# Kernel optimization log

Hardware: AMD Instinct MI355X
Metric: run time of the kernel (lower is better)

Reference implementation:

```python
import jax, jax.numpy as jnp
import numpy as np

N_NODES = 50000
N_EDGES = 1000000
H_DIM = 128
OUT_DIM = 64
N_RELS = 16  # num_bases == num_rels


def setup_inputs() -> dict:
    key = jax.random.key(0)
    ks = jax.random.split(key, 12)
    node_ids = jnp.arange(N_NODES, dtype=jnp.int64) if jax.config.jax_enable_x64 else jnp.arange(N_NODES, dtype=jnp.int32)
    src = jax.random.randint(ks[0], (N_EDGES,), 0, N_NODES)
    dst = jax.random.randint(ks[1], (N_EDGES,), 0, N_NODES)
    etype = jax.random.randint(ks[2], (N_EDGES,), 0, N_RELS)
    norm = jax.random.uniform(ks[3], (N_EDGES, 1), dtype=jnp.float32)
    s1 = 1.0 / np.sqrt(H_DIM)
    s2 = 1.0 / np.sqrt(OUT_DIM)
    emb = jax.random.normal(ks[4], (N_NODES, H_DIM), dtype=jnp.float32)
    V1 = jax.random.normal(ks[5], (N_RELS, H_DIM, H_DIM), dtype=jnp.float32) * s1
    comp1 = jax.random.normal(ks[6], (N_RELS, N_RELS), dtype=jnp.float32) * (1.0 / np.sqrt(N_RELS))
    bias1 = jnp.zeros((H_DIM,), dtype=jnp.float32)
    V2 = jax.random.normal(ks[7], (N_RELS, H_DIM, OUT_DIM), dtype=jnp.float32) * s2
    comp2 = jax.random.normal(ks[8], (N_RELS, N_RELS), dtype=jnp.float32) * (1.0 / np.sqrt(N_RELS))
    bias2 = jnp.zeros((OUT_DIM,), dtype=jnp.float32)
    return {"node_ids": node_ids, "src": src, "dst": dst, "etype": etype, "norm": norm,
            "emb": emb, "V1": V1, "comp1": comp1, "bias1": bias1,
            "V2": V2, "comp2": comp2, "bias2": bias2}


def _rel_graph_conv(x, src, dst, etype, norm, V, comp, bias, num_nodes):
    # Basis decomposition: W_r = sum_b comp[r, b] * V_b  -> [R, in, out]
    W = jnp.einsum('rb,bio->rio', comp, V)
    # Per-relation transform of all nodes: [R, N, out]
    Y = jnp.einsum('ni,rio->rno', x, W)
    # Per-edge message: gather (etype, src) then scale by norm  -> [E, out]
    m = Y[etype, src] * norm
    # Scatter-add to destination nodes
    h = jax.ops.segment_sum(m, dst, num_segments=num_nodes)
    return h + bias


def reference(node_ids, src, dst, etype, norm, emb, V1, comp1, bias1, V2, comp2, bias2):
    x = emb[node_ids]  # [N, H]
    h = jax.nn.relu(_rel_graph_conv(x, src, dst, etype, norm, V1, comp1, bias1, x.shape[0]))
    h = _rel_graph_conv(h, src, dst, etype, norm, V2, comp2, bias2, x.shape[0])
    return h
```

## Files before the change

kernel.cpp:

```cpp
#include <hip/hip_runtime.h>


typedef short bf16x8 __attribute__((ext_vector_type(8)));
typedef float f32x4 __attribute__((ext_vector_type(4)));

#define RELS 16
#define HDIM 128
#define DSTBLK 66
#define MT_P 5
#define CHUNK 32
#define MAXBINS 12288
#define MAXCH 96

__device__ inline unsigned short f2bf(float f) {
  unsigned int u = __float_as_uint(f);
  unsigned int r = u + 0x7FFFu + ((u >> 16) & 1u);
  return (unsigned short)(r >> 16);
}

__device__ inline void barrier_nodrain() {
  __builtin_amdgcn_sched_barrier(0);
  asm volatile("s_waitcnt lgkmcnt(0)" ::: "memory");
  __builtin_amdgcn_s_barrier();
  __builtin_amdgcn_sched_barrier(0);
}

__global__ void cvt_bf16(const float* __restrict__ in, unsigned short* __restrict__ out, int n8) {
  int i = blockIdx.x * blockDim.x + threadIdx.x;
  if (i >= n8) return;
  float4 a = ((const float4*)in)[i * 2];
  float4 b = ((const float4*)in)[i * 2 + 1];
  uint4 o;
  o.x = (unsigned)f2bf(a.x) | ((unsigned)f2bf(a.y) << 16);
  o.y = (unsigned)f2bf(a.z) | ((unsigned)f2bf(a.w) << 16);
  o.z = (unsigned)f2bf(b.x) | ((unsigned)f2bf(b.y) << 16);
  o.w = (unsigned)f2bf(b.z) | ((unsigned)f2bf(b.w) << 16);
  ((uint4*)out)[i] = o;
}

__global__ void compute_w(const float* __restrict__ comp, const float* __restrict__ V,
                          unsigned short* __restrict__ Wt, int IO) {
  int idx = blockIdx.x * blockDim.x + threadIdx.x;
  if (idx >= RELS * IO * HDIM) return;
  int k = idx & (HDIM - 1);
  int o = (idx >> 7) % IO;
  int r = idx / (IO * HDIM);
  float s = 0.f;
#pragma unroll
  for (int b = 0; b < RELS; b++)
    s = fmaf(comp[r * RELS + b], V[(size_t)b * HDIM * IO + (size_t)k * IO + o], s);
  Wt[idx] = f2bf(s);
}

__global__ void hist_bins(const int* __restrict__ dst, const int* __restrict__ etype,
                          int n, int nbins, int* __restrict__ counts) {
  __shared__ int lh[MAXBINS];
  for (int j = threadIdx.x; j < nbins; j += blockDim.x) lh[j] = 0;
  __syncthreads();
  for (int i = blockIdx.x * blockDim.x + threadIdx.x; i < n; i += gridDim.x * blockDim.x)
    atomicAdd(&lh[(dst[i] / DSTBLK) * RELS + etype[i]], 1);
  __syncthreads();
  for (int j = threadIdx.x; j < nbins; j += blockDim.x) {
    int c = lh[j];
    if (c) atomicAdd(&counts[j], c);
  }
}

__global__ void scan_offsets(const int* __restrict__ counts, int* __restrict__ offsets, int nbins) {
  __shared__ int csum[256];
  const int t = threadIdx.x;
  const int CH = (nbins + 255) / 256;
  int lo = t * CH, hi = min(lo + CH, nbins);
  int s = 0;
  for (int i = lo; i < hi; i++) s += (counts[i] + 15) & ~15;
  csum[t] = s;
  __syncthreads();
#pragma unroll
  for (int d = 1; d < 256; d <<= 1) {
    int v = (t >= d) ? csum[t - d] : 0;
    __syncthreads();
    csum[t] += v;
    __syncthreads();
  }
  int run = (t == 0) ? 0 : csum[t - 1];
  for (int i = lo; i < hi; i++) {
    offsets[i] = run;
    run += (counts[i] + 15) & ~15;
  }
  if (lo < nbins && hi == nbins) offsets[nbins] = run;
}

__global__ void scatter_bins(const int* __restrict__ src, const int* __restrict__ dst,
                             const int* __restrict__ etype, const float* __restrict__ norm,
                             int n, const int* __restrict__ offsets, int* __restrict__ cursor,
                             uint2* __restrict__ ebuf) {
  for (int i = blockIdx.x * blockDim.x + threadIdx.x; i < n; i += gridDim.x * blockDim.x) {
    int d = dst[i];
    int blk = d / DSTBLK;
    int b = blk * RELS + etype[i];
    int p = offsets[b] + atomicAdd(&cursor[b], 1);
    ebuf[p] = make_uint2((unsigned)src[i] | ((unsigned)(d - blk * DSTBLK) << 20),
                         __float_as_uint(norm[i]));
  }
}

template <int OUT, bool BF16_RELU_OUT>
__launch_bounds__(256, (OUT == 64) ? 4 : 3)
__global__ void rgcn_layer(const unsigned short* __restrict__ Xb,
                           const unsigned short* __restrict__ Wt,
                           const uint2* __restrict__ ebuf,
                           const int* __restrict__ offsets, const int* __restrict__ counts,
                           const float* __restrict__ bias, void* __restrict__ Hout,
                           int nNodes) {
  constexpr int NT = OUT / 64;
  __shared__ __align__(16) unsigned short xs[2][CHUNK][136];
  __shared__ __align__(16) unsigned short ys[OUT][40];
  __shared__ __align__(16) unsigned short pmat[2][80][40];
  __shared__ __align__(8) int2 descS[MAXCH];
  __shared__ int sBase[16], sCnt[16], sStart[17];

  const int t = threadIdx.x;
  const int w = t >> 6;
  const int lane = t & 63;
  const int quad = lane >> 4;
  const int l16 = lane & 15;
  const int r0 = t >> 4;
  const int k8 = t & 15;
  const bool isHandler = (t & 7) == 0;
  const int myCol = t >> 3;
  const int nodeBase = blockIdx.x * DSTBLK;
  const int binBase = blockIdx.x * RELS;
  const int colBase = w * (OUT / 4);

  for (int i = t; i < 2 * CHUNK * 136 / 8; i += 256) ((uint4*)xs)[i] = make_uint4(0, 0, 0, 0);
  for (int i = t; i < OUT * 40 / 8; i += 256) ((uint4*)ys)[i] = make_uint4(0, 0, 0, 0);
  for (int i = t; i < 2 * 80 * 40 / 8; i += 256) ((uint4*)pmat)[i] = make_uint4(0, 0, 0, 0);

  if (t < 16) {
    sBase[t] = offsets[binBase + t];
    sCnt[t] = counts[binBase + t];
  }
  __syncthreads();
  if (t == 0) {
    int run = 0;
#pragma unroll
    for (int b = 0; b < 16; b++) {
      sStart[b] = run;
      run += (sCnt[b] + CHUNK - 1) / CHUNK;
    }
    sStart[16] = min(run, MAXCH);
  }
  __syncthreads();
  if (t < 16) {
    int st = sStart[t], ba = sBase[t], c = sCnt[t];
    for (int j = 0; j * CHUNK < c; j++)
      if (st + j < MAXCH)
        descS[st + j] = make_int2(ba + j * CHUNK, min(CHUNK, c - j * CHUNK) | (t << 8));
  }
  __syncthreads();
  const int nCh = sStart[16];

  f32x4 pacc[MT_P][NT] = {};

  struct Pipe {
    uint2 E0, E1;
    uint4 G0, G1;
    uint2 H;
  };
  Pipe P, Q;
  int pd0 = -1, pd1 = -1;
  int n1 = 0, n2 = 0;

  if (nCh > 0) {
    int2 d0 = descS[0];
    int2 d1 = (nCh > 1) ? descS[1] : make_int2(0, 0);
    int2 d2 = (nCh > 2) ? descS[2] : make_int2(0, 0);
    const int rows0 = d0.y & 0xFF;
    n1 = d1.y & 0xFF;
    n2 = d2.y & 0xFF;
    uint2 a0, a1, am, e10, e11;
    if (r0 < rows0) a0 = ebuf[d0.x + r0];
    if (16 + r0 < rows0) a1 = ebuf[d0.x + 16 + r0];
    if (isHandler && myCol < rows0) am = ebuf[d0.x + myCol];
    if (r0 < n1) e10 = ebuf[d1.x + r0];
    if (16 + r0 < n1) e11 = ebuf[d1.x + 16 + r0];
    if (isHandler && myCol < n1) Q.H = ebuf[d1.x + myCol];
    if (r0 < n2) Q.E0 = ebuf[d2.x + r0];
    if (16 + r0 < n2) Q.E1 = ebuf[d2.x + 16 + r0];
    if (r0 < rows0)
      *(uint4*)&xs[0][r0][k8 * 8] =
          *(const uint4*)(Xb + (size_t)(a0.x & 0xFFFFFu) * HDIM + k8 * 8);
    if (16 + r0 < rows0)
      *(uint4*)&xs[0][16 + r0][k8 * 8] =
          *(const uint4*)(Xb + (size_t)(a1.x & 0xFFFFFu) * HDIM + k8 * 8);
    if (isHandler && myCol < rows0) {
      int dl = (int)(am.x >> 20) & 127;
      pmat[0][dl][myCol] = f2bf(__uint_as_float(am.y));
      pd0 = dl;
    }
    if (r0 < n1) Q.G0 = *(const uint4*)(Xb + (size_t)(e10.x & 0xFFFFFu) * HDIM + k8 * 8);
    if (16 + r0 < n1) Q.G1 = *(const uint4*)(Xb + (size_t)(e11.x & 0xFFFFFu) * HDIM + k8 * 8);
  }
  barrier_nodrain();

  int curRel = -1;
  bf16x8 wf[4][NT];

  auto phase = [&](int ci, int cbv, Pipe& in, Pipe& out, int n1v, int n2v,
                   int& pdW) -> int {
    int2 dc = descS[ci];
    const int nRows = dc.y & 0xFF;
    const int rel = dc.y >> 8;

    if (rel != curRel) {
      curRel = rel;
      const unsigned short* Wr = Wt + (size_t)rel * OUT * HDIM;
#pragma unroll
      for (int ks = 0; ks < 4; ks++)
#pragma unroll
        for (int nt = 0; nt < NT; nt++)
          wf[ks][nt] = *(const bf16x8*)(Wr + (size_t)(colBase + nt * 16 + l16) * HDIM + ks * 32 + quad * 8);
    }

    int2 d3 = (ci + 3 < nCh) ? descS[ci + 3] : make_int2(0, 0);
    const int n3 = d3.y & 0xFF;
    if (r0 < n3) out.E0 = ebuf[d3.x + r0];
    if (16 + r0 < n3) out.E1 = ebuf[d3.x + 16 + r0];
    if (isHandler && myCol < n2v) out.H = ebuf[descS[ci + 2].x + myCol];

#pragma unroll
    for (int mt = 0; mt < 2; mt++) {
      if (mt * 16 < nRows) {
        f32x4 dacc[NT] = {};
        __builtin_amdgcn_s_setprio(1);
#pragma unroll
        for (int ks = 0; ks < 4; ks++) {
          bf16x8 a = *(const bf16x8*)&xs[cbv][mt * 16 + l16][ks * 32 + quad * 8];
#pragma unroll
          for (int nt = 0; nt < NT; nt++)
            dacc[nt] = __builtin_amdgcn_mfma_f32_16x16x32_bf16(a, wf[ks][nt], dacc[nt], 0, 0, 0);
        }
        __builtin_amdgcn_s_setprio(0);
#pragma unroll
        for (int nt = 0; nt < NT; nt++) {
          uint2 pk;
          pk.x = (unsigned)f2bf(dacc[nt][0]) | ((unsigned)f2bf(dacc[nt][1]) << 16);
          pk.y = (unsigned)f2bf(dacc[nt][2]) | ((unsigned)f2bf(dacc[nt][3]) << 16);
          *(uint2*)&ys[colBase + nt * 16 + l16][mt * 16 + quad * 4] = pk;
        }
      }
    }

    if (r0 < n2v) out.G0 = *(const uint4*)(Xb + (size_t)(in.E0.x & 0xFFFFFu) * HDIM + k8 * 8);
    if (16 + r0 < n2v) out.G1 = *(const uint4*)(Xb + (size_t)(in.E1.x & 0xFFFFFu) * HDIM + k8 * 8);

    {
      bf16x8 bfv[NT];
#pragma unroll
      for (int nt = 0; nt < NT; nt++)
        bfv[nt] = *(const bf16x8*)&ys[colBase + nt * 16 + l16][quad * 8];
      __builtin_amdgcn_s_setprio(1);
#pragma unroll
      for (int mt = 0; mt < MT_P; mt++) {
        bf16x8 a = *(const bf16x8*)&pmat[cbv][mt * 16 + l16][quad * 8];
#pragma unroll
        for (int nt = 0; nt < NT; nt++)
          pacc[mt][nt] = __builtin_amdgcn_mfma_f32_16x16x32_bf16(a, bfv[nt], pacc[mt][nt], 0, 0, 0);
      }
      __builtin_amdgcn_s_setprio(0);
    }

    if (r0 < n1v) *(uint4*)&xs[cbv ^ 1][r0][k8 * 8] = in.G0;
    if (16 + r0 < n1v) *(uint4*)&xs[cbv ^ 1][16 + r0][k8 * 8] = in.G1;
    if (isHandler) {
      if (pdW >= 0) pmat[cbv ^ 1][pdW][myCol] = 0;
      if (myCol < n1v) {
        int dl = (int)(in.H.x >> 20) & 127;
        pmat[cbv ^ 1][dl][myCol] = f2bf(__uint_as_float(in.H.y));
        pdW = dl;
      } else {
        pdW = -1;
      }
    }

    if (ci + 1 < nCh) barrier_nodrain();
    return n3;
  };

  int ci = 0;
  while (ci < nCh) {
    int n3 = phase(ci, 0, Q, P, n1, n2, pd1);
    n1 = n2; n2 = n3; ci++;
    if (ci >= nCh) break;
    n3 = phase(ci, 1, P, Q, n1, n2, pd0);
    n1 = n2; n2 = n3; ci++;
  }

#pragma unroll
  for (int mt = 0; mt < MT_P; mt++) {
#pragma unroll
    for (int reg = 0; reg < 4; reg++) {
      int ld = mt * 16 + quad * 4 + reg;
      int node = nodeBase + ld;
      if (ld < DSTBLK && node < nNodes) {
#pragma unroll
        for (int nt = 0; nt < NT; nt++) {
          int col = colBase + nt * 16 + l16;
          float v = pacc[mt][nt][reg] + bias[col];
          if constexpr (BF16_RELU_OUT)
            ((unsigned short*)Hout)[(size_t)node * OUT + col] = f2bf(fmaxf(v, 0.f));
          else
            ((float*)Hout)[(size_t)node * OUT + col] = v;
        }
      }
    }
  }
}

extern "C" void kernel_launch(void* const* d_in, const int* in_sizes, int n_in,
                              void* d_out, int out_size, void* d_ws, size_t ws_size,
                              hipStream_t stream) {
  const int*   src   = (const int*)d_in[1];
  const int*   dst   = (const int*)d_in[2];
  const int*   etype = (const int*)d_in[3];
  const float* norm  = (const float*)d_in[4];
  const float* emb   = (const float*)d_in[5];
  const float* V1    = (const float*)d_in[6];
  const float* comp1 = (const float*)d_in[7];
  const float* bias1 = (const float*)d_in[8];
  const float* V2    = (const float*)d_in[9];
  const float* comp2 = (const float*)d_in[10];
  const float* bias2 = (const float*)d_in[11];
  float* out = (float*)d_out;

  const int N = in_sizes[0];
  const int E = in_sizes[1];
  const int H = 128, O = 64;
  const int NB = (N + DSTBLK - 1) / DSTBLK;
  const int NBINS = NB * RELS;
  const int EPAD_MAX = E + NBINS * 16;

  char* ws = (char*)d_ws;
  size_t off = 0;
  auto alloc = [&](size_t bytes) -> void* {
    void* p = ws + off;
    off += (bytes + 255) & ~(size_t)255;
    return p;
  };
  unsigned short* W1t  = (unsigned short*)alloc(sizeof(short) * RELS * H * H);
  unsigned short* W2t  = (unsigned short*)alloc(sizeof(short) * RELS * O * H);
  unsigned short* embh = (unsigned short*)alloc(sizeof(short) * (size_t)N * H);
  unsigned short* h1b  = (unsigned short*)alloc(sizeof(short) * (size_t)N * H);
  uint2* ebuf = (uint2*)alloc(sizeof(uint2) * EPAD_MAX);
  int* counts  = (int*)alloc(sizeof(int) * NBINS);
  int* cursor  = (int*)alloc(sizeof(int) * NBINS);
  int* offsets = (int*)alloc(sizeof(int) * (NBINS + 1));

  hipMemsetAsync(counts, 0, sizeof(int) * NBINS, stream);
  hipMemsetAsync(cursor, 0, sizeof(int) * NBINS, stream);

  cvt_bf16<<<((size_t)N * H / 8 + 255) / 256, 256, 0, stream>>>(emb, embh, N * H / 8);
  compute_w<<<(RELS * H * H + 255) / 256, 256, 0, stream>>>(comp1, V1, W1t, H);
  compute_w<<<(RELS * O * H + 255) / 256, 256, 0, stream>>>(comp2, V2, W2t, O);
  hist_bins<<<256, 256, 0, stream>>>(dst, etype, E, NBINS, counts);
  scan_offsets<<<1, 256, 0, stream>>>(counts, offsets, NBINS);
  scatter_bins<<<1024, 256, 0, stream>>>(src, dst, etype, norm, E, offsets, cursor, ebuf);

  rgcn_layer<128, true><<<NB, 256, 0, stream>>>(embh, W1t, ebuf, offsets, counts, bias1, (void*)h1b, N);
  rgcn_layer<64, false><<<NB, 256, 0, stream>>>(h1b, W2t, ebuf, offsets, counts, bias2, (void*)out, N);
}
```

Before: 428.7 us.

## Keep per-relation transform in registers instead of LDS round-trip

Stops staging the bf16 per-edge transform result through the shared-memory ys buffer. The MFMA accumulators from the first GEMM are packed straight into B-operand registers with the hardware v_cvt_pk_bf16_f32 instruction. The pmat column index is permuted (hslot) so the edge ordering matches the register layout of the accumulator fragments. This removes LDS writes and reads plus a layout dependency, and lets the OUT=128 variant request 4 waves per SIMD, which risks register spills.

```diff
diff --git a/kernel.cpp b/kernel.cpp
--- a/kernel.cpp
+++ b/kernel.cpp
@@ -16,6 +16,12 @@
   unsigned int u = __float_as_uint(f);
   unsigned int r = u + 0x7FFFu + ((u >> 16) & 1u);
   return (unsigned short)(r >> 16);
+}
+
+__device__ inline unsigned cvtpk(float lo, float hi) {
+  unsigned r;
+  asm("v_cvt_pk_bf16_f32 %0, %1, %2" : "=v"(r) : "v"(lo), "v"(hi));
+  return r;
 }
 
 __device__ inline void barrier_nodrain() {
@@ -105,7 +111,7 @@
 }
 
 template <int OUT, bool BF16_RELU_OUT>
-__launch_bounds__(256, (OUT == 64) ? 4 : 3)
+__launch_bounds__(256, 4)
 __global__ void rgcn_layer(const unsigned short* __restrict__ Xb,
                            const unsigned short* __restrict__ Wt,
                            const uint2* __restrict__ ebuf,
@@ -114,7 +120,6 @@
                            int nNodes) {
   constexpr int NT = OUT / 64;
   __shared__ __align__(16) unsigned short xs[2][CHUNK][136];
-  __shared__ __align__(16) unsigned short ys[OUT][40];
   __shared__ __align__(16) unsigned short pmat[2][80][40];
   __shared__ __align__(8) int2 descS[MAXCH];
   __shared__ int sBase[16], sCnt[16], sStart[17];
@@ -128,12 +133,12 @@
   const int k8 = t & 15;
   const bool isHandler = (t & 7) == 0;
   const int myCol = t >> 3;
+  const int hslot = ((myCol >> 2) & 3) * 8 + ((myCol >> 4) & 1) * 4 + (myCol & 3);
   const int nodeBase = blockIdx.x * DSTBLK;
   const int binBase = blockIdx.x * RELS;
   const int colBase = w * (OUT / 4);
 
   for (int i = t; i < 2 * CHUNK * 136 / 8; i += 256) ((uint4*)xs)[i] = make_uint4(0, 0, 0, 0);
-  for (int i = t; i < OUT * 40 / 8; i += 256) ((uint4*)ys)[i] = make_uint4(0, 0, 0, 0);
   for (int i = t; i < 2 * 80 * 40 / 8; i += 256) ((uint4*)pmat)[i] = make_uint4(0, 0, 0, 0);
 
   if (t < 16) {
@@ -195,7 +200,7 @@
           *(const uint4*)(Xb + (size_t)(a1.x & 0xFFFFFu) * HDIM + k8 * 8);
     if (isHandler && myCol < rows0) {
       int dl = (int)(am.x >> 20) & 127;
-      pmat[0][dl][myCol] = f2bf(__uint_as_float(am.y));
+      pmat[0][dl][hslot] = f2bf(__uint_as_float(am.y));
       pd0 = dl;
     }
     if (r0 < n1) Q.G0 = *(const uint4*)(Xb + (size_t)(e10.x & 0xFFFFFu) * HDIM + k8 * 8);
@@ -228,26 +233,19 @@
     if (16 + r0 < n3) out.E1 = ebuf[d3.x + 16 + r0];
     if (isHandler && myCol < n2v) out.H = ebuf[descS[ci + 2].x + myCol];
 
+    f32x4 dacc[2][NT] = {};
 #pragma unroll
     for (int mt = 0; mt < 2; mt++) {
       if (mt * 16 < nRows) {
-        f32x4 dacc[NT] = {};
         __builtin_amdgcn_s_setprio(1);
 #pragma unroll
         for (int ks = 0; ks < 4; ks++) {
           bf16x8 a = *(const bf16x8*)&xs[cbv][mt * 16 + l16][ks * 32 + quad * 8];
 #pragma unroll
           for (int nt = 0; nt < NT; nt++)
-            dacc[nt] = __builtin_amdgcn_mfma_f32_16x16x32_bf16(a, wf[ks][nt], dacc[nt], 0, 0, 0);
+            dacc[mt][nt] = __builtin_amdgcn_mfma_f32_16x16x32_bf16(a, wf[ks][nt], dacc[mt][nt], 0, 0, 0);
         }
         __builtin_amdgcn_s_setprio(0);
-#pragma unroll
-        for (int nt = 0; nt < NT; nt++) {
-          uint2 pk;
-          pk.x = (unsigned)f2bf(dacc[nt][0]) | ((unsigned)f2bf(dacc[nt][1]) << 16);
-          pk.y = (unsigned)f2bf(dacc[nt][2]) | ((unsigned)f2bf(dacc[nt][3]) << 16);
-          *(uint2*)&ys[colBase + nt * 16 + l16][mt * 16 + quad * 4] = pk;
-        }
       }
     }
 
@@ -257,8 +255,14 @@
     {
       bf16x8 bfv[NT];
 #pragma unroll
-      for (int nt = 0; nt < NT; nt++)
-        bfv[nt] = *(const bf16x8*)&ys[colBase + nt * 16 + l16][quad * 8];
+      for (int nt = 0; nt < NT; nt++) {
+        uint4 bw;
+        bw.x = cvtpk(dacc[0][nt][0], dacc[0][nt][1]);
+        bw.y = cvtpk(dacc[0][nt][2], dacc[0][nt][3]);
+        bw.z = cvtpk(dacc[1][nt][0], dacc[1][nt][1]);
+        bw.w = cvtpk(dacc[1][nt][2], dacc[1][nt][3]);
+        bfv[nt] = *(bf16x8*)&bw;
+      }
       __builtin_amdgcn_s_setprio(1);
 #pragma unroll
       for (int mt = 0; mt < MT_P; mt++) {
@@ -273,10 +277,10 @@
     if (r0 < n1v) *(uint4*)&xs[cbv ^ 1][r0][k8 * 8] = in.G0;
     if (16 + r0 < n1v) *(uint4*)&xs[cbv ^ 1][16 + r0][k8 * 8] = in.G1;
     if (isHandler) {
-      if (pdW >= 0) pmat[cbv ^ 1][pdW][myCol] = 0;
+      if (pdW >= 0) pmat[cbv ^ 1][pdW][hslot] = 0;
       if (myCol < n1v) {
         int dl = (int)(in.H.x >> 20) & 127;
-        pmat[cbv ^ 1][dl][myCol] = f2bf(__uint_as_float(in.H.y));
+        pmat[cbv ^ 1][dl][hslot] = f2bf(__uint_as_float(in.H.y));
         pdW = dl;
       } else {
         pdW = -1;
```

After: 490.2 us. 1.14x slower.
